# Performance work log

Measured on AMD Instinct MI355X. Metric: run time of the kernel, lower is better.

Reference implementation:

```python
import jax, jax.numpy as jnp
import numpy as np


def setup_inputs() -> dict:
    key = jax.random.key(0)
    k1, k2 = jax.random.split(key)
    x = jax.random.normal(k1, (131072, 256), dtype=jnp.float32)
    centroids = jax.random.normal(k2, (2048, 256), dtype=jnp.float32)
    return {"x": x, "centroids": centroids}


def reference(x, centroids):
    """One k-means step: L2 nearest-centroid assignment + scatter-mean update.

    x:         (n, d) sample vectors
    centroids: (K, d) current centroids
    returns:   (K, d) new centroids
    """
    K = centroids.shape[0]
    # Squared L2 distance argmin; ||x||^2 term is constant per row, drop it.
    # scores[n, K] = ||c_k||^2 - 2 * x_n . c_k
    c_sq = jnp.sum(centroids * centroids, axis=-1)          # (K,)
    scores = c_sq[None, :] - 2.0 * jnp.einsum("nd,kd->nk", x, centroids)
    assigns = jnp.argmin(scores, axis=-1)                    # (n,) int
    # Segment mean update; keep old centroid for empty clusters.
    sums = jax.ops.segment_sum(x, assigns, num_segments=K)   # (K, d)
    counts = jax.ops.segment_sum(jnp.ones((x.shape[0],), x.dtype), assigns,
                                 num_segments=K)             # (K,)
    nonempty = counts > 0
    means = sums / jnp.maximum(counts, 1.0)[:, None]
    new_centroids = jnp.where(nonempty[:, None], means, centroids)
    return new_centroids
```

## Files before the change

kernel.cpp:

```cpp
#include <hip/hip_runtime.h>

typedef unsigned short u16;
typedef unsigned int u32;
typedef unsigned long long u64;
typedef __attribute__((ext_vector_type(4)))  int  i32x4;
typedef __attribute__((ext_vector_type(16))) int  i32x16;
typedef __attribute__((ext_vector_type(16))) char i8x16;

#define NPTS 131072
#define DIM  256
#define KC   2048

constexpr float S1  = 0.0625f;
constexpr float S2  = S1 / 254.0f;
constexpr float S3  = S2 * S2 / S1;
constexpr float IS1 = 16.0f;
constexpr float IS2 = 4064.0f;
constexpr float IS3 = 1.0f / S3;
constexpr float W_A = S1 * S1;
constexpr float R2  = 1.0f / 254.0f;

__device__ inline void quant3(float v, char& q1, char& q2, char& q3) {
    float a = fminf(fmaxf(rintf(v * IS1), -127.f), 127.f);
    float r1 = fmaf(-a, S1, v);
    float b = rintf(r1 * IS2);
    float r2 = fmaf(-b, S2, r1);
    float c = rintf(r2 * IS3);
    q1 = (char)a; q2 = (char)b; q3 = (char)c;
}

#define GLD16(gsrc, ldst) \
    __builtin_amdgcn_global_load_lds( \
        (const __attribute__((address_space(1))) void*)(gsrc), \
        (__attribute__((address_space(3))) void*)(ldst), 16, 0, 0)

__global__ void cprep_kernel(const float* __restrict__ cen,
                             char* __restrict__ c_q,
                             int* __restrict__ c_sqi,
                             int* __restrict__ hist,
                             float* __restrict__ sums) {
    if (blockIdx.x < 8) hist[blockIdx.x * 256 + threadIdx.x] = 0;
    ((float4*)sums)[blockIdx.x * 256 + threadIdx.x] = (float4){0.f, 0.f, 0.f, 0.f};
    const int lane = threadIdx.x & 63;
    const int wv   = threadIdx.x >> 6;
    const int n    = blockIdx.x * 4 + wv;
    float4 v = ((const float4*)(cen + (size_t)n * DIM))[lane];
    float ss = v.x * v.x + v.y * v.y + v.z * v.z + v.w * v.w;
    float fv[4] = {v.x, v.y, v.z, v.w};
    char q1[4], q2[4], q3[4];
#pragma unroll
    for (int j = 0; j < 4; ++j) quant3(fv[j], q1[j], q2[j], q3[j]);
    const int g = n >> 5, r32 = n & 31;
    const int s = lane >> 2;
    const size_t base = ((size_t)((g * 16 + s) * 32 + r32)) * 16 + (lane & 3) * 4;
    u32 p1 = (u32)(unsigned char)q1[0] | ((u32)(unsigned char)q1[1] << 8) |
             ((u32)(unsigned char)q1[2] << 16) | ((u32)(unsigned char)q1[3] << 24);
    u32 p2 = (u32)(unsigned char)q2[0] | ((u32)(unsigned char)q2[1] << 8) |
             ((u32)(unsigned char)q2[2] << 16) | ((u32)(unsigned char)q2[3] << 24);
    u32 p3 = (u32)(unsigned char)q3[0] | ((u32)(unsigned char)q3[1] << 8) |
             ((u32)(unsigned char)q3[2] << 16) | ((u32)(unsigned char)q3[3] << 24);
    *(u32*)(c_q + base) = p1;
    *(u32*)(c_q + (size_t)KC * DIM + base) = p2;
    *(u32*)(c_q + (size_t)2 * KC * DIM + base) = p3;
#pragma unroll
    for (int off = 32; off > 0; off >>= 1) ss += __shfl_xor(ss, off);
    if (lane == 0) c_sqi[n] = (int)rintf(ss * (0.5f * 254.0f / W_A));
}

__global__ __launch_bounds__(256, 3) void assign_kernel(
    const float* __restrict__ x, const char* __restrict__ c_q,
    const int* __restrict__ c_sqi, int* __restrict__ assigns,
    int* __restrict__ hist) {
    __shared__ char lds_c[3 * 12288 + 8192];

    {
        const int phase = (blockIdx.x >> 8) % 3;
        for (int i = 0; i < phase * 7; ++i) __builtin_amdgcn_s_sleep(4);
    }

    const int tid  = threadIdx.x;
    const int lane = tid & 63;
    const int wv   = tid >> 6;
    const int l31  = lane & 31;
    const int kh   = lane >> 5;

    const char* cl1 = c_q;
    const char* cl2 = c_q + (size_t)KC * DIM;
    const char* cl3 = c_q + (size_t)2 * KC * DIM;

    GLD16((const char*)c_sqi + tid * 16,         lds_c + 36864 + tid * 16);
    GLD16((const char*)c_sqi + (tid + 256) * 16, lds_c + 36864 + (tid + 256) * 16);
    GLD16(cl1 + tid * 16,        lds_c + tid * 16);
    GLD16(cl2 + tid * 16,        lds_c + 4096 + tid * 16);
    GLD16(cl3 + tid * 16,        lds_c + 8192 + tid * 16);
    GLD16(cl1 + 4096 + tid * 16, lds_c + 12288 + tid * 16);
    GLD16(cl2 + 4096 + tid * 16, lds_c + 12288 + 4096 + tid * 16);
    GLD16(cl3 + 4096 + tid * 16, lds_c + 12288 + 8192 + tid * 16);

    const int m = blockIdx.x * 128 + wv * 32 + l31;
    const float4* xr = (const float4*)(x + (size_t)m * DIM);
    i8x16 xq1[8], xq2[8], xq3[8];
#pragma unroll
    for (int kt = 0; kt < 8; ++kt) {
        float tmp[16];
#pragma unroll
        for (int j = 0; j < 4; ++j) {
            float4 f = xr[kt * 8 + kh * 4 + j];
            tmp[j * 4 + 0] = f.x; tmp[j * 4 + 1] = f.y;
            tmp[j * 4 + 2] = f.z; tmp[j * 4 + 3] = f.w;
        }
        i8x16 v1, v2, v3;
#pragma unroll
        for (int j = 0; j < 16; ++j) {
            char a, b, c;
            quant3(tmp[j], a, b, c);
            v1[j] = a; v2[j] = b; v3[j] = c;
        }
        xq1[kt] = v1; xq2[kt] = v2; xq3[kt] = v3;
    }

    float best = 3.4e38f;
    int bidx = 0;
    int b3 = 0;

    const int* csqL = (const int*)(lds_c + 36864);

    for (int t = 0; t < 64; ++t) {
        i32x16 accA = {}, accB = {}, accC = {};
#pragma unroll
        for (int h2 = 0; h2 < 2; ++h2) {
            if (t == 63 && h2 == 1) {
                asm volatile("s_waitcnt vmcnt(0)" ::: "memory");
            } else {
                asm volatile("s_waitcnt vmcnt(3)" ::: "memory");
            }
            __builtin_amdgcn_s_barrier();
            __builtin_amdgcn_sched_barrier(0);
            if (2 * t + h2 + 2 < 128) {
                int pn = b3 + 2; if (pn >= 3) pn -= 3;
                char* d = lds_c + pn * 12288;
                const size_t so = (size_t)(2 * t + h2 + 2) * 4096;
                GLD16(cl1 + so + tid * 16, d + tid * 16);
                GLD16(cl2 + so + tid * 16, d + 4096 + tid * 16);
                GLD16(cl3 + so + tid * 16, d + 8192 + tid * 16);
            }
            const char* cb = lds_c + b3 * 12288;
            __builtin_amdgcn_s_setprio(1);
#pragma unroll
            for (int kt2 = 0; kt2 < 4; ++kt2) {
                const int off = kt2 * 1024 + kh * 512 + l31 * 16;
                i32x4 c1 = __builtin_bit_cast(i32x4, *(const i8x16*)(cb + off));
                i32x4 c2 = __builtin_bit_cast(i32x4, *(const i8x16*)(cb + 4096 + off));
                i32x4 c3 = __builtin_bit_cast(i32x4, *(const i8x16*)(cb + 8192 + off));
                i32x4 x1 = __builtin_bit_cast(i32x4, xq1[h2 * 4 + kt2]);
                i32x4 x2 = __builtin_bit_cast(i32x4, xq2[h2 * 4 + kt2]);
                i32x4 x3 = __builtin_bit_cast(i32x4, xq3[h2 * 4 + kt2]);
                accA = __builtin_amdgcn_mfma_i32_32x32x32_i8(c1, x1, accA, 0, 0, 0);
                accB = __builtin_amdgcn_mfma_i32_32x32x32_i8(c1, x2, accB, 0, 0, 0);
                accC = __builtin_amdgcn_mfma_i32_32x32x32_i8(c2, x2, accC, 0, 0, 0);
                accB = __builtin_amdgcn_mfma_i32_32x32x32_i8(c2, x1, accB, 0, 0, 0);
                accC = __builtin_amdgcn_mfma_i32_32x32x32_i8(c1, x3, accC, 0, 0, 0);
                accC = __builtin_amdgcn_mfma_i32_32x32x32_i8(c3, x1, accC, 0, 0, 0);
            }
            __builtin_amdgcn_s_setprio(0);
            b3 += 1; if (b3 == 3) b3 = 0;
        }

#pragma unroll
        for (int bq = 0; bq < 4; ++bq) {
            int4 cs = *(const int4*)(csqL + (t * 8 + 2 * bq + kh) * 4);
            const int n0 = t * 32 + 8 * bq + 4 * kh;
            int csa[4] = {cs.x, cs.y, cs.z, cs.w};
#pragma unroll
            for (int r = 0; r < 4; ++r) {
                const int idx = bq * 4 + r;
                int D  = __mul24(accA[idx], 254) + accB[idx];
                int Vi = csa[r] - D;
                float v = fmaf((float)accC[idx], -R2, (float)Vi);
                if (v < best) { best = v; bidx = n0 + r; }
            }
        }
    }

    float oval = __shfl_xor(best, 32);
    int   oidx = __shfl_xor(bidx, 32);
    if (oval < best || (oval == best && oidx < bidx)) { best = oval; bidx = oidx; }
    if (lane < 32) {
        assigns[m] = bidx;
        atomicAdd(&hist[bidx], 1);
    }
}

__global__ void scan_kernel(const int* __restrict__ hist,
                            int* __restrict__ base_,
                            int* __restrict__ cursor) {
    __shared__ int tmp[256];
    const int tid = threadIdx.x;
    int v[8], s = 0;
#pragma unroll
    for (int j = 0; j < 8; ++j) { v[j] = hist[tid * 8 + j]; s += v[j]; }
    tmp[tid] = s;
    __syncthreads();
    for (int off = 1; off < 256; off <<= 1) {
        int t = (tid >= off) ? tmp[tid - off] : 0;
        __syncthreads();
        tmp[tid] += t;
        __syncthreads();
    }
    int ex = tmp[tid] - s;
#pragma unroll
    for (int j = 0; j < 8; ++j) {
        base_[tid * 8 + j] = ex;
        cursor[tid * 8 + j] = ex;
        ex += v[j];
    }
}

__global__ void reorder_kernel(const int* __restrict__ assigns,
                               int* __restrict__ cursor,
                               int* __restrict__ order) {
    const int p = blockIdx.x * 256 + threadIdx.x;
    const int a = assigns[p];
    int pos = atomicAdd(&cursor[a], 1);
    order[pos] = p;
}

__global__ void reduce_kernel(const float* __restrict__ x,
                              const int* __restrict__ order,
                              const int* __restrict__ assigns,
                              float* __restrict__ sums) {
    const int tid = threadIdx.x;
    const int r0 = blockIdx.x * 256;
    float acc = 0.f;
    int cur = assigns[order[r0]];
    for (int r = 0; r < 256; r += 4) {
        int p0 = order[r0 + r + 0], p1 = order[r0 + r + 1];
        int p2 = order[r0 + r + 2], p3 = order[r0 + r + 3];
        float v0 = x[(size_t)p0 * DIM + tid];
        float v1 = x[(size_t)p1 * DIM + tid];
        float v2 = x[(size_t)p2 * DIM + tid];
        float v3 = x[(size_t)p3 * DIM + tid];
        int a0 = assigns[p0], a1 = assigns[p1], a2 = assigns[p2], a3 = assigns[p3];
        if (a0 != cur) { unsafeAtomicAdd(&sums[(size_t)cur * DIM + tid], acc); acc = 0.f; cur = a0; }
        acc += v0;
        if (a1 != cur) { unsafeAtomicAdd(&sums[(size_t)cur * DIM + tid], acc); acc = 0.f; cur = a1; }
        acc += v1;
        if (a2 != cur) { unsafeAtomicAdd(&sums[(size_t)cur * DIM + tid], acc); acc = 0.f; cur = a2; }
        acc += v2;
        if (a3 != cur) { unsafeAtomicAdd(&sums[(size_t)cur * DIM + tid], acc); acc = 0.f; cur = a3; }
        acc += v3;
    }
    unsafeAtomicAdd(&sums[(size_t)cur * DIM + tid], acc);
}

__global__ void finalize_kernel(const float* __restrict__ sums,
                                const int* __restrict__ hist,
                                const float* __restrict__ cen,
                                float* __restrict__ out) {
    const int id = blockIdx.x * 256 + threadIdx.x;
    const int k = id >> 6;
    const int cnt = hist[k];
    float4 s = ((const float4*)sums)[id];
    float4 c = ((const float4*)cen)[id];
    float4 o;
    if (cnt > 0) {
        float r = 1.0f / (float)cnt;
        o.x = s.x * r; o.y = s.y * r; o.z = s.z * r; o.w = s.w * r;
    } else {
        o = c;
    }
    ((float4*)out)[id] = o;
}

extern "C" void kernel_launch(void* const* d_in, const int* in_sizes, int n_in,
                              void* d_out, int out_size, void* d_ws, size_t ws_size,
                              hipStream_t stream) {
    (void)in_sizes; (void)n_in; (void)out_size; (void)ws_size;
    const float* x   = (const float*)d_in[0];
    const float* cen = (const float*)d_in[1];
    float* out = (float*)d_out;

    char* ws = (char*)d_ws;
    size_t off = 0;
    char* c_q = (char*)(ws + off);           off += (size_t)3 * KC * DIM;
    int* c_sqi = (int*)(ws + off);           off += (size_t)KC * 4;
    int* assigns = (int*)(ws + off);         off += (size_t)NPTS * 4;
    int* hist = (int*)(ws + off);            off += (size_t)KC * 4;
    int* base_ = (int*)(ws + off);           off += (size_t)KC * 4;
    int* cursor = (int*)(ws + off);          off += (size_t)KC * 4;
    int* order = (int*)(ws + off);           off += (size_t)NPTS * 4;
    float* sums = (float*)(ws + off);        off += (size_t)KC * DIM * 4;

    cprep_kernel<<<KC / 4, 256, 0, stream>>>(cen, c_q, c_sqi, hist, sums);
    assign_kernel<<<NPTS / 128, 256, 0, stream>>>(x, c_q, c_sqi, assigns, hist);
    scan_kernel<<<1, 256, 0, stream>>>(hist, base_, cursor);
    reorder_kernel<<<NPTS / 256, 256, 0, stream>>>(assigns, cursor, order);
    reduce_kernel<<<NPTS / 256, 256, 0, stream>>>(x, order, assigns, sums);
    finalize_kernel<<<KC * 64 / 256, 256, 0, stream>>>(sums, hist, cen, out);
}
```

Measured before the change: 607.6 us.

## Switch assign kernel to 16x16x64 int8 MFMA with 512-thread blocks

The centroid assignment GEMM moves from 32x32x32 to 16x16x64 int8 MFMA tiles. Centroid quantized data is re-laid out in cprep to match the new operand shape. Blocks grow to 512 threads, each wave handling 16 points, with larger 32-centroid LDS stages triple-buffered per iteration. The staggered start sleep is removed. This halves the number of barrier/wait steps and shrinks accumulator registers, but doubles the centroid LDS reads per point and changes occupancy.

```diff
diff --git a/kernel.cpp b/kernel.cpp
--- a/kernel.cpp
+++ b/kernel.cpp
@@ -4,7 +4,6 @@
 typedef unsigned int u32;
 typedef unsigned long long u64;
 typedef __attribute__((ext_vector_type(4)))  int  i32x4;
-typedef __attribute__((ext_vector_type(16))) int  i32x16;
 typedef __attribute__((ext_vector_type(16))) char i8x16;
 
 #define NPTS 131072
@@ -50,9 +49,11 @@
     char q1[4], q2[4], q3[4];
 #pragma unroll
     for (int j = 0; j < 4; ++j) quant3(fv[j], q1[j], q2[j], q3[j]);
-    const int g = n >> 5, r32 = n & 31;
-    const int s = lane >> 2;
-    const size_t base = ((size_t)((g * 16 + s) * 32 + r32)) * 16 + (lane & 3) * 4;
+    const int g16 = n >> 4, c = n & 15;
+    const int kc  = lane >> 4;
+    const int kq  = (lane >> 2) & 3;
+    const size_t base = ((size_t)((g16 * 4 + kc) * 64 + kq * 16 + c)) * 16
+                        + (lane & 3) * 4;
     u32 p1 = (u32)(unsigned char)q1[0] | ((u32)(unsigned char)q1[1] << 8) |
              ((u32)(unsigned char)q1[2] << 16) | ((u32)(unsigned char)q1[3] << 24);
     u32 p2 = (u32)(unsigned char)q2[0] | ((u32)(unsigned char)q2[1] << 8) |
@@ -67,47 +68,41 @@
     if (lane == 0) c_sqi[n] = (int)rintf(ss * (0.5f * 254.0f / W_A));
 }
 
-__global__ __launch_bounds__(256, 3) void assign_kernel(
+__global__ __launch_bounds__(512, 4) void assign_kernel(
     const float* __restrict__ x, const char* __restrict__ c_q,
     const int* __restrict__ c_sqi, int* __restrict__ assigns,
     int* __restrict__ hist) {
-    __shared__ char lds_c[3 * 12288 + 8192];
-
-    {
-        const int phase = (blockIdx.x >> 8) % 3;
-        for (int i = 0; i < phase * 7; ++i) __builtin_amdgcn_s_sleep(4);
-    }
+    __shared__ char lds_c[3 * 24576 + 8192];
 
     const int tid  = threadIdx.x;
     const int lane = tid & 63;
     const int wv   = tid >> 6;
-    const int l31  = lane & 31;
-    const int kh   = lane >> 5;
+    const int p16  = lane & 15;
+    const int kq   = lane >> 4;
 
     const char* cl1 = c_q;
     const char* cl2 = c_q + (size_t)KC * DIM;
     const char* cl3 = c_q + (size_t)2 * KC * DIM;
 
-    GLD16((const char*)c_sqi + tid * 16,         lds_c + 36864 + tid * 16);
-    GLD16((const char*)c_sqi + (tid + 256) * 16, lds_c + 36864 + (tid + 256) * 16);
+    GLD16((const char*)c_sqi + tid * 16, lds_c + 73728 + tid * 16);
     GLD16(cl1 + tid * 16,        lds_c + tid * 16);
-    GLD16(cl2 + tid * 16,        lds_c + 4096 + tid * 16);
-    GLD16(cl3 + tid * 16,        lds_c + 8192 + tid * 16);
-    GLD16(cl1 + 4096 + tid * 16, lds_c + 12288 + tid * 16);
-    GLD16(cl2 + 4096 + tid * 16, lds_c + 12288 + 4096 + tid * 16);
-    GLD16(cl3 + 4096 + tid * 16, lds_c + 12288 + 8192 + tid * 16);
-
-    const int m = blockIdx.x * 128 + wv * 32 + l31;
+    GLD16(cl2 + tid * 16,        lds_c + 8192 + tid * 16);
+    GLD16(cl3 + tid * 16,        lds_c + 16384 + tid * 16);
+    GLD16(cl1 + 8192 + tid * 16, lds_c + 24576 + tid * 16);
+    GLD16(cl2 + 8192 + tid * 16, lds_c + 24576 + 8192 + tid * 16);
+    GLD16(cl3 + 8192 + tid * 16, lds_c + 24576 + 16384 + tid * 16);
+
+    const int m = blockIdx.x * 128 + wv * 16 + p16;
     const float4* xr = (const float4*)(x + (size_t)m * DIM);
-    i8x16 xq1[8], xq2[8], xq3[8];
-#pragma unroll
-    for (int kt = 0; kt < 8; ++kt) {
+    i8x16 xq1[4], xq2[4], xq3[4];
+#pragma unroll
+    for (int kc = 0; kc < 4; ++kc) {
         float tmp[16];
 #pragma unroll
-        for (int j = 0; j < 4; ++j) {
-            float4 f = xr[kt * 8 + kh * 4 + j];
-            tmp[j * 4 + 0] = f.x; tmp[j * 4 + 1] = f.y;
-            tmp[j * 4 + 2] = f.z; tmp[j * 4 + 3] = f.w;
+        for (int j4 = 0; j4 < 4; ++j4) {
+            float4 f = xr[kc * 16 + kq * 4 + j4];
+            tmp[j4 * 4 + 0] = f.x; tmp[j4 * 4 + 1] = f.y;
+            tmp[j4 * 4 + 2] = f.z; tmp[j4 * 4 + 3] = f.w;
         }
         i8x16 v1, v2, v3;
 #pragma unroll
@@ -116,76 +111,92 @@
             quant3(tmp[j], a, b, c);
             v1[j] = a; v2[j] = b; v3[j] = c;
         }
-        xq1[kt] = v1; xq2[kt] = v2; xq3[kt] = v3;
+        xq1[kc] = v1; xq2[kc] = v2; xq3[kc] = v3;
     }
 
     float best = 3.4e38f;
     int bidx = 0;
     int b3 = 0;
-
-    const int* csqL = (const int*)(lds_c + 36864);
+    const int* csqL = (const int*)(lds_c + 73728);
 
     for (int t = 0; t < 64; ++t) {
-        i32x16 accA = {}, accB = {}, accC = {};
-#pragma unroll
-        for (int h2 = 0; h2 < 2; ++h2) {
-            if (t == 63 && h2 == 1) {
-                asm volatile("s_waitcnt vmcnt(0)" ::: "memory");
-            } else {
-                asm volatile("s_waitcnt vmcnt(3)" ::: "memory");
+        if (t == 63) {
+            asm volatile("s_waitcnt vmcnt(0)" ::: "memory");
+        } else {
+            asm volatile("s_waitcnt vmcnt(3)" ::: "memory");
+        }
+        __builtin_amdgcn_s_barrier();
+        __builtin_amdgcn_sched_barrier(0);
+        if (t + 2 < 64) {
+            int pn = b3 + 2; if (pn >= 3) pn -= 3;
+            char* d = lds_c + pn * 24576;
+            const size_t so = (size_t)(t + 2) * 8192;
+            GLD16(cl1 + so + tid * 16, d + tid * 16);
+            GLD16(cl2 + so + tid * 16, d + 8192 + tid * 16);
+            GLD16(cl3 + so + tid * 16, d + 16384 + tid * 16);
+        }
+        const char* cb = lds_c + b3 * 24576;
+        i32x4 accA0 = {}, accB0 = {}, accC0 = {};
+        i32x4 accA1 = {}, accB1 = {}, accC1 = {};
+        __builtin_amdgcn_s_setprio(1);
+#pragma unroll
+        for (int kc = 0; kc < 4; ++kc) {
+            const int off = kc * 1024 + lane * 16;
+            i32x4 c1a = __builtin_bit_cast(i32x4, *(const i8x16*)(cb + off));
+            i32x4 c2a = __builtin_bit_cast(i32x4, *(const i8x16*)(cb + 8192 + off));
+            i32x4 c3a = __builtin_bit_cast(i32x4, *(const i8x16*)(cb + 16384 + off));
+            i32x4 c1b = __builtin_bit_cast(i32x4, *(const i8x16*)(cb + 4096 + off));
+            i32x4 c2b = __builtin_bit_cast(i32x4, *(const i8x16*)(cb + 12288 + off));
+            i32x4 c3b = __builtin_bit_cast(i32x4, *(const i8x16*)(cb + 20480 + off));
+            i32x4 x1 = __builtin_bit_cast(i32x4, xq1[kc]);
+            i32x4 x2 = __builtin_bit_cast(i32x4, xq2[kc]);
+            i32x4 x3 = __builtin_bit_cast(i32x4, xq3[kc]);
+            accA0 = __builtin_amdgcn_mfma_i32_16x16x64_i8(c1a, x1, accA0, 0, 0, 0);
+            accA1 = __builtin_amdgcn_mfma_i32_16x16x64_i8(c1b, x1, accA1, 0, 0, 0);
+            accB0 = __builtin_amdgcn_mfma_i32_16x16x64_i8(c1a, x2, accB0, 0, 0, 0);
+            accB1 = __builtin_amdgcn_mfma_i32_16x16x64_i8(c1b, x2, accB1, 0, 0, 0);
+            accC0 = __builtin_amdgcn_mfma_i32_16x16x64_i8(c2a, x2, accC0, 0, 0, 0);
+            accC1 = __builtin_amdgcn_mfma_i32_16x16x64_i8(c2b, x2, accC1, 0, 0, 0);
+            accB0 = __builtin_amdgcn_mfma_i32_16x16x64_i8(c2a, x1, accB0, 0, 0, 0);
+            accB1 = __builtin_amdgcn_mfma_i32_16x16x64_i8(c2b, x1, accB1, 0, 0, 0);
+            accC0 = __builtin_amdgcn_mfma_i32_16x16x64_i8(c1a, x3, accC0, 0, 0, 0);
+            accC1 = __builtin_amdgcn_mfma_i32_16x16x64_i8(c1b, x3, accC1, 0, 0, 0);
+            accC0 = __builtin_amdgcn_mfma_i32_16x16x64_i8(c3a, x1, accC0, 0, 0, 0);
+            accC1 = __builtin_amdgcn_mfma_i32_16x16x64_i8(c3b, x1, accC1, 0, 0, 0);
+        }
+        __builtin_amdgcn_s_setprio(0);
+        b3 += 1; if (b3 == 3) b3 = 0;
+
+        {
+            int4 cs0 = *(const int4*)(csqL + t * 32 + kq * 4);
+            int4 cs1 = *(const int4*)(csqL + t * 32 + 16 + kq * 4);
+            const int n0 = t * 32 + kq * 4;
+            int csa0[4] = {cs0.x, cs0.y, cs0.z, cs0.w};
+            int csa1[4] = {cs1.x, cs1.y, cs1.z, cs1.w};
+#pragma unroll
+            for (int r = 0; r < 4; ++r) {
+                int D0 = __mul24(accA0[r], 254) + accB0[r];
+                float v0 = fmaf((float)accC0[r], -R2, (float)(csa0[r] - D0));
+                if (v0 < best) { best = v0; bidx = n0 + r; }
             }
-            __builtin_amdgcn_s_barrier();
-            __builtin_amdgcn_sched_barrier(0);
-            if (2 * t + h2 + 2 < 128) {
-                int pn = b3 + 2; if (pn >= 3) pn -= 3;
-                char* d = lds_c + pn * 12288;
-                const size_t so = (size_t)(2 * t + h2 + 2) * 4096;
-                GLD16(cl1 + so + tid * 16, d + tid * 16);
-                GLD16(cl2 + so + tid * 16, d + 4096 + tid * 16);
-                GLD16(cl3 + so + tid * 16, d + 8192 + tid * 16);
+#pragma unroll
+            for (int r = 0; r < 4; ++r) {
+                int D1 = __mul24(accA1[r], 254) + accB1[r];
+                float v1 = fmaf((float)accC1[r], -R2, (float)(csa1[r] - D1));
+                if (v1 < best) { best = v1; bidx = n0 + 16 + r; }
             }
-            const char* cb = lds_c + b3 * 12288;
-            __builtin_amdgcn_s_setprio(1);
-#pragma unroll
-            for (int kt2 = 0; kt2 < 4; ++kt2) {
-                const int off = kt2 * 1024 + kh * 512 + l31 * 16;
-                i32x4 c1 = __builtin_bit_cast(i32x4, *(const i8x16*)(cb + off));
-                i32x4 c2 = __builtin_bit_cast(i32x4, *(const i8x16*)(cb + 4096 + off));
-                i32x4 c3 = __builtin_bit_cast(i32x4, *(const i8x16*)(cb + 8192 + off));
-                i32x4 x1 = __builtin_bit_cast(i32x4, xq1[h2 * 4 + kt2]);
-                i32x4 x2 = __builtin_bit_cast(i32x4, xq2[h2 * 4 + kt2]);
-                i32x4 x3 = __builtin_bit_cast(i32x4, xq3[h2 * 4 + kt2]);
-                accA = __builtin_amdgcn_mfma_i32_32x32x32_i8(c1, x1, accA, 0, 0, 0);
-                accB = __builtin_amdgcn_mfma_i32_32x32x32_i8(c1, x2, accB, 0, 0, 0);
-                accC = __builtin_amdgcn_mfma_i32_32x32x32_i8(c2, x2, accC, 0, 0, 0);
-                accB = __builtin_amdgcn_mfma_i32_32x32x32_i8(c2, x1, accB, 0, 0, 0);
-                accC = __builtin_amdgcn_mfma_i32_32x32x32_i8(c1, x3, accC, 0, 0, 0);
-                accC = __builtin_amdgcn_mfma_i32_32x32x32_i8(c3, x1, accC, 0, 0, 0);
-            }
-            __builtin_amdgcn_s_setprio(0);
-            b3 += 1; if (b3 == 3) b3 = 0;
-        }
-
-#pragma unroll
-        for (int bq = 0; bq < 4; ++bq) {
-            int4 cs = *(const int4*)(csqL + (t * 8 + 2 * bq + kh) * 4);
-            const int n0 = t * 32 + 8 * bq + 4 * kh;
-            int csa[4] = {cs.x, cs.y, cs.z, cs.w};
-#pragma unroll
-            for (int r = 0; r < 4; ++r) {
-                const int idx = bq * 4 + r;
-                int D  = __mul24(accA[idx], 254) + accB[idx];
-                int Vi = csa[r] - D;
-                float v = fmaf((float)accC[idx], -R2, (float)Vi);
-                if (v < best) { best = v; bidx = n0 + r; }
-            }
-        }
-    }
-
-    float oval = __shfl_xor(best, 32);
-    int   oidx = __shfl_xor(bidx, 32);
-    if (oval < best || (oval == best && oidx < bidx)) { best = oval; bidx = oidx; }
-    if (lane < 32) {
+        }
+    }
+
+    {
+        float oval = __shfl_xor(best, 16);
+        int   oidx = __shfl_xor(bidx, 16);
+        if (oval < best || (oval == best && oidx < bidx)) { best = oval; bidx = oidx; }
+        oval = __shfl_xor(best, 32);
+        oidx = __shfl_xor(bidx, 32);
+        if (oval < best || (oval == best && oidx < bidx)) { best = oval; bidx = oidx; }
+    }
+    if (lane < 16) {
         assigns[m] = bidx;
         atomicAdd(&hist[bidx], 1);
     }
@@ -292,7 +303,7 @@
     float* sums = (float*)(ws + off);        off += (size_t)KC * DIM * 4;
 
     cprep_kernel<<<KC / 4, 256, 0, stream>>>(cen, c_q, c_sqi, hist, sums);
-    assign_kernel<<<NPTS / 128, 256, 0, stream>>>(x, c_q, c_sqi, assigns, hist);
+    assign_kernel<<<NPTS / 128, 512, 0, stream>>>(x, c_q, c_sqi, assigns, hist);
     scan_kernel<<<1, 256, 0, stream>>>(hist, base_, cursor);
     reorder_kernel<<<NPTS / 256, 256, 0, stream>>>(assigns, cursor, order);
     reduce_kernel<<<NPTS / 256, 256, 0, stream>>>(x, order, assigns, sums);
```

Result: faster. 571.2 us, median of 2 (-6.0%).
